# Kernel tuning notes

Hardware: AMD Instinct MI355X
Metric: run time of the kernel (lower is better)

## Reference

```python
import jax, jax.numpy as jnp
import numpy as np

N = 35709   # vertices
F = 70789   # triangles
B = 64
CAMERA_DISTANCE = 10.0
FOCAL = 1015.0
IMAGE_SIZE = 224

SH_A = (np.pi, 2 * np.pi / np.sqrt(3.0), 2 * np.pi / np.sqrt(8.0))
SH_C = (1 / np.sqrt(4 * np.pi), np.sqrt(3.0) / np.sqrt(4 * np.pi), 3 * np.sqrt(5.0) / np.sqrt(12 * np.pi))


def _persc_proj():
    center = IMAGE_SIZE / 2
    m = np.array([FOCAL, 0, center, 0, FOCAL, center, 0, 0, 1], dtype=np.float32).reshape(3, 3).T
    return jnp.asarray(m)


def setup_inputs() -> dict:
    key = jax.random.key(0)
    ks = jax.random.split(key, 9)
    return {
        "coeffs": jax.random.normal(ks[0], (B, 257), jnp.float32),
        "meanshape": jax.random.normal(ks[1], (3 * N,), jnp.float32),
        "idBase": jax.random.normal(ks[2], (3 * N, 80), jnp.float32),
        "exBase": jax.random.normal(ks[3], (3 * N, 64), jnp.float32),
        "meantex": jax.random.uniform(ks[4], (3 * N,), jnp.float32) * 255.0,
        "texBase": jax.random.normal(ks[5], (3 * N, 80), jnp.float32),
        "persc_proj": _persc_proj(),
        "init_lit": jnp.array([0.8, 0, 0, 0, 0, 0, 0, 0, 0], jnp.float32).reshape(1, 1, 9),
        "point_buf": jax.random.randint(ks[6], (N, 8), 0, F + 1),   # index F = zero-pad row
        "face_buf": jax.random.randint(ks[7], (F, 3), 0, N),
        "keypoints": jax.random.randint(ks[8], (68,), 0, N),
    }


def _l2norm(x):
    # matches torch F.normalize(p=2, eps=1e-12)
    return x / jnp.maximum(jnp.linalg.norm(x, axis=-1, keepdims=True), 1e-12)


def _rotation(angles):
    x, y, z = angles[:, 0], angles[:, 1], angles[:, 2]
    o, zr = jnp.ones_like(x), jnp.zeros_like(x)
    cx, sx = jnp.cos(x), jnp.sin(x)
    cy, sy = jnp.cos(y), jnp.sin(y)
    cz, sz = jnp.cos(z), jnp.sin(z)
    rx = jnp.stack([o, zr, zr, zr, cx, -sx, zr, sx, cx], -1).reshape(-1, 3, 3)
    ry = jnp.stack([cy, zr, sy, zr, o, zr, -sy, zr, cy], -1).reshape(-1, 3, 3)
    rz = jnp.stack([cz, -sz, zr, sz, cz, zr, zr, zr, o], -1).reshape(-1, 3, 3)
    return jnp.transpose(rz @ ry @ rx, (0, 2, 1))


def _compute_norm(face_shape, face_buf, point_buf):
    tri = face_shape[:, face_buf]                 # (B, F, 3verts, 3xyz) gather
    e1 = tri[:, :, 0] - tri[:, :, 1]
    e2 = tri[:, :, 1] - tri[:, :, 2]
    fn = _l2norm(jnp.cross(e1, e2))               # (B, F, 3)
    fn = jnp.concatenate([fn, jnp.zeros((fn.shape[0], 1, 3), fn.dtype)], axis=1)
    vn = jnp.sum(fn[:, point_buf], axis=2)        # (B, N, 3) gather-sum over 8 faces
    return _l2norm(vn)


def _compute_color(face_texture, face_norm, gamma, init_lit):
    a, c = SH_A, SH_C
    g = gamma.reshape(gamma.shape[0], 3, 9) + init_lit   # (B, 3, 9)
    g = jnp.transpose(g, (0, 2, 1))                      # (B, 9, 3)
    nx, ny, nz = face_norm[..., 0:1], face_norm[..., 1:2], face_norm[..., 2:3]
    Y = jnp.concatenate([
        a[0] * c[0] * jnp.ones_like(nx),
        -a[1] * c[1] * ny,
        a[1] * c[1] * nz,
        -a[1] * c[1] * nx,
        a[2] * c[2] * nx * ny,
        -a[2] * c[2] * ny * nz,
        0.5 * a[2] * c[2] / np.sqrt(3.0) * (3 * nz ** 2 - 1),
        -a[2] * c[2] * nx * nz,
        0.5 * a[2] * c[2] * (nx ** 2 - ny ** 2)], axis=-1)   # (B, N, 9)
    rgb = jnp.einsum('bnk,bkc->bnc', Y, g)
    return rgb * face_texture


def reference(coeffs, meanshape, idBase, exBase, meantex, texBase, persc_proj, init_lit, point_buf, face_buf, keypoints):
    id_c, ex_c, tex_c = coeffs[:, 0:80], coeffs[:, 80:144], coeffs[:, 144:224]
    angles, gamma, trans = coeffs[:, 224:227], coeffs[:, 227:254], coeffs[:, 254:257]
    Bsz = coeffs.shape[0]
    # shape blending (dense GEMMs)
    shape_flat = (jnp.einsum('ij,aj->ai', idBase, id_c)
                  + jnp.einsum('ij,aj->ai', exBase, ex_c)
                  + meanshape[None])
    face_shape = shape_flat.reshape(Bsz, -1, 3)
    rot = _rotation(angles)
    face_shape_t = face_shape @ rot + trans[:, None, :]
    # to camera: z -> camera_distance - z
    face_vertex = jnp.concatenate([face_shape_t[..., :2], CAMERA_DISTANCE - face_shape_t[..., 2:]], axis=-1)
    # perspective projection
    proj = face_vertex @ persc_proj
    face_proj = proj[..., :2] / proj[..., 2:]
    landmark = face_proj[:, keypoints, :]
    # texture blending
    face_texture = ((jnp.einsum('ij,aj->ai', texBase, tex_c) + meantex[None]) / 255.0).reshape(Bsz, -1, 3)
    # mesh normals on untransformed shape, rotated into camera frame
    face_norm = _compute_norm(face_shape, face_buf, point_buf)
    face_norm_r = face_norm @ rot
    face_color = _compute_color(face_texture, face_norm_r, gamma, init_lit)
    return face_vertex, face_color, landmark
```

## Files before the change

kernel.cpp:

```cpp
#include <hip/hip_runtime.h>

#define N_V 35709
#define N_F 70789
#define NR  (3*N_V)
#define NB  64

#define WS_ROT    0
#define WS_GM     576
#define WS_CTRS   2304
#define WS_CTRT   11520
#define WS_SHAPET 16640

__global__ __launch_bounds__(64) void k_setup_rot(
    const float* __restrict__ coeffs, const float* __restrict__ init_lit,
    float* __restrict__ rotM, float* __restrict__ gm)
{
    int b = threadIdx.x;
    const float* cb = coeffs + b * 257;

    float ax = cb[224], ay = cb[225], az = cb[226];
    float cx = cosf(ax), sx = sinf(ax);
    float cy = cosf(ay), sy = sinf(ay);
    float cz = cosf(az), sz = sinf(az);
    float m[9];
    m[0] = cz * cy;
    m[1] = cz * sy * sx - sz * cx;
    m[2] = sz * sx + cz * sy * cx;
    m[3] = sz * cy;
    m[4] = cz * cx + sz * sy * sx;
    m[5] = sz * sy * cx - cz * sx;
    m[6] = -sy;
    m[7] = cy * sx;
    m[8] = cy * cx;
#pragma unroll
    for (int k = 0; k < 9; k++) rotM[b * 9 + k] = m[k];

#pragma unroll
    for (int k = 0; k < 9; k++) {
        float il = init_lit[k];
#pragma unroll
        for (int c = 0; c < 3; c++)
            gm[b * 27 + k * 3 + c] = cb[227 + c * 9 + k] + il;
    }
}

__global__ __launch_bounds__(64) void k_transpose(
    const float* __restrict__ coeffs,
    float* __restrict__ ctrS, float* __restrict__ ctrT)
{
    int j = blockIdx.x;
    int b = threadIdx.x;
    float v = coeffs[b * 257 + j];
    if (j < 144) ctrS[j * 64 + b] = v;
    else         ctrT[(j - 144) * 64 + b] = v;
}

__global__ __launch_bounds__(256) void k_gemm(
    const float* __restrict__ idBase, const float* __restrict__ exBase,
    const float* __restrict__ texBase, const float* __restrict__ meanshape,
    const float* __restrict__ meantex,
    const float* __restrict__ ctrS, const float* __restrict__ ctrT,
    float* __restrict__ shapeT,
    float* __restrict__ texT,
    int tex_transposed)
{
    __shared__ float tsh[4][64 * 33];
    int w    = threadIdx.x >> 6;
    int lane = threadIdx.x & 63;
    int h    = blockIdx.y;
    int i0w  = blockIdx.x * 256 + w * 64;
    int i    = i0w + lane;
    int iv   = (i < NR) ? i : (NR - 1);
    float* sh = tsh[w];

    float acc[32];

#pragma unroll
    for (int c = 0; c < 32; c++) acc[c] = 0.f;
    {
        const float4* r4 = (const float4*)(idBase + (size_t)iv * 80);
#pragma unroll 2
        for (int jq = 0; jq < 20; jq++) {
            float4 a4 = r4[jq];
            float as[4] = {a4.x, a4.y, a4.z, a4.w};
#pragma unroll
            for (int s = 0; s < 4; s++) {
                float a = as[s];
                const float4* cp = (const float4*)(ctrS + (jq * 4 + s) * 64 + h * 32);
#pragma unroll
                for (int q = 0; q < 8; q++) {
                    float4 c = cp[q];
                    acc[4 * q + 0] += a * c.x;
                    acc[4 * q + 1] += a * c.y;
                    acc[4 * q + 2] += a * c.z;
                    acc[4 * q + 3] += a * c.w;
                }
            }
        }
        const float4* e4 = (const float4*)(exBase + (size_t)iv * 64);
#pragma unroll 2
        for (int jq = 0; jq < 16; jq++) {
            float4 a4 = e4[jq];
            float as[4] = {a4.x, a4.y, a4.z, a4.w};
#pragma unroll
            for (int s = 0; s < 4; s++) {
                float a = as[s];
                const float4* cp = (const float4*)(ctrS + (80 + jq * 4 + s) * 64 + h * 32);
#pragma unroll
                for (int q = 0; q < 8; q++) {
                    float4 c = cp[q];
                    acc[4 * q + 0] += a * c.x;
                    acc[4 * q + 1] += a * c.y;
                    acc[4 * q + 2] += a * c.z;
                    acc[4 * q + 3] += a * c.w;
                }
            }
        }
        float ms = meanshape[iv];
#pragma unroll
        for (int c = 0; c < 32; c++) sh[lane * 33 + c] = acc[c] + ms;
#pragma unroll 4
        for (int it = 0; it < 32; it++) {
            int r  = it * 2 + (lane >> 5);
            int cb = lane & 31;
            int rg = i0w + r;
            float v = sh[r * 33 + cb];
            if (rg < NR) shapeT[(size_t)rg * 64 + h * 32 + cb] = v;
        }
    }

#pragma unroll
    for (int c = 0; c < 32; c++) acc[c] = 0.f;
    {
        const float4* t4 = (const float4*)(texBase + (size_t)iv * 80);
#pragma unroll 2
        for (int jq = 0; jq < 20; jq++) {
            float4 a4 = t4[jq];
            float as[4] = {a4.x, a4.y, a4.z, a4.w};
#pragma unroll
            for (int s = 0; s < 4; s++) {
                float a = as[s];
                const float4* cp = (const float4*)(ctrT + (jq * 4 + s) * 64 + h * 32);
#pragma unroll
                for (int q = 0; q < 8; q++) {
                    float4 c = cp[q];
                    acc[4 * q + 0] += a * c.x;
                    acc[4 * q + 1] += a * c.y;
                    acc[4 * q + 2] += a * c.z;
                    acc[4 * q + 3] += a * c.w;
                }
            }
        }
        float mt = meantex[iv];
        const float inv255 = 1.0f / 255.0f;
        if (tex_transposed) {
#pragma unroll
            for (int c = 0; c < 32; c++) sh[lane * 33 + c] = (acc[c] + mt) * inv255;
#pragma unroll 4
            for (int it = 0; it < 32; it++) {
                int r  = it * 2 + (lane >> 5);
                int cb = lane & 31;
                int rg = i0w + r;
                float v = sh[r * 33 + cb];
                if (rg < NR) texT[(size_t)rg * 64 + h * 32 + cb] = v;
            }
        } else {
            if (i < NR) {
#pragma unroll
                for (int c = 0; c < 32; c++)
                    texT[(size_t)(h * 32 + c) * NR + i] = (acc[c] + mt) * inv255;
            }
        }
    }
}

__global__ __launch_bounds__(256) void k_repack3(
    const float* __restrict__ shapeT, float* __restrict__ shape3)
{
    int wave = threadIdx.x >> 6;
    int b    = threadIdx.x & 63;
    int v0   = blockIdx.x * 32 + wave * 8;
#pragma unroll
    for (int r = 0; r < 8; r++) {
        int v = v0 + r;
        if (v < N_V) {
            float x = shapeT[(size_t)(3 * v)     * 64 + b];
            float y = shapeT[(size_t)(3 * v + 1) * 64 + b];
            float z = shapeT[(size_t)(3 * v + 2) * 64 + b];
            float* o = shape3 + ((size_t)v * 64 + b) * 3;
            o[0] = x; o[1] = y; o[2] = z;
        }
    }
}

__global__ __launch_bounds__(256) void k_facenorm3(
    const float* __restrict__ shape3,
    const int* __restrict__ face_buf,
    float* __restrict__ fnT3)
{
    int wave = threadIdx.x >> 6;
    int b    = threadIdx.x & 63;
    int f0   = blockIdx.x * 32 + wave * 8;
#pragma unroll
    for (int fr = 0; fr < 8; fr++) {
        int f = f0 + fr;
        if (f < N_F) {
            int i0 = face_buf[f * 3 + 0];
            int i1 = face_buf[f * 3 + 1];
            int i2 = face_buf[f * 3 + 2];
            const float* p0 = shape3 + ((size_t)i0 * 64 + b) * 3;
            const float* p1 = shape3 + ((size_t)i1 * 64 + b) * 3;
            const float* p2 = shape3 + ((size_t)i2 * 64 + b) * 3;
            float p0x = p0[0], p0y = p0[1], p0z = p0[2];
            float p1x = p1[0], p1y = p1[1], p1z = p1[2];
            float p2x = p2[0], p2y = p2[1], p2z = p2[2];
            float e1x = p0x - p1x, e1y = p0y - p1y, e1z = p0z - p1z;
            float e2x = p1x - p2x, e2y = p1y - p2y, e2z = p1z - p2z;
            float ccx = e1y * e2z - e1z * e2y;
            float ccy = e1z * e2x - e1x * e2z;
            float ccz = e1x * e2y - e1y * e2x;
            float l = sqrtf(ccx * ccx + ccy * ccy + ccz * ccz);
            float inv = 1.0f / fmaxf(l, 1e-12f);
            float* o = fnT3 + ((size_t)f * 64 + b) * 3;
            o[0] = ccx * inv; o[1] = ccy * inv; o[2] = ccz * inv;
        } else if (f == N_F) {
            float* o = fnT3 + ((size_t)f * 64 + b) * 3;
            o[0] = 0.f; o[1] = 0.f; o[2] = 0.f;
        }
    }
}

__global__ __launch_bounds__(256) void k_facenorm(
    const float* __restrict__ shapeT,
    const int* __restrict__ face_buf,
    float* __restrict__ fnT3)
{
    int wave = threadIdx.x >> 6;
    int b    = threadIdx.x & 63;
    int f0   = blockIdx.x * 32 + wave * 8;
#pragma unroll
    for (int fr = 0; fr < 8; fr++) {
        int f = f0 + fr;
        if (f < N_F) {
            int i0 = face_buf[f * 3 + 0];
            int i1 = face_buf[f * 3 + 1];
            int i2 = face_buf[f * 3 + 2];
            float p0x = shapeT[(size_t)(3 * i0)     * 64 + b];
            float p0y = shapeT[(size_t)(3 * i0 + 1) * 64 + b];
            float p0z = shapeT[(size_t)(3 * i0 + 2) * 64 + b];
            float p1x = shapeT[(size_t)(3 * i1)     * 64 + b];
            float p1y = shapeT[(size_t)(3 * i1 + 1) * 64 + b];
            float p1z = shapeT[(size_t)(3 * i1 + 2) * 64 + b];
            float p2x = shapeT[(size_t)(3 * i2)     * 64 + b];
            float p2y = shapeT[(size_t)(3 * i2 + 1) * 64 + b];
            float p2z = shapeT[(size_t)(3 * i2 + 2) * 64 + b];
            float e1x = p0x - p1x, e1y = p0y - p1y, e1z = p0z - p1z;
            float e2x = p1x - p2x, e2y = p1y - p2y, e2z = p1z - p2z;
            float ccx = e1y * e2z - e1z * e2y;
            float ccy = e1z * e2x - e1x * e2z;
            float ccz = e1x * e2y - e1y * e2x;
            float l = sqrtf(ccx * ccx + ccy * ccy + ccz * ccz);
            float inv = 1.0f / fmaxf(l, 1e-12f);
            float* o = fnT3 + ((size_t)f * 64 + b) * 3;
            o[0] = ccx * inv; o[1] = ccy * inv; o[2] = ccz * inv;
        } else if (f == N_F) {
            float* o = fnT3 + ((size_t)f * 64 + b) * 3;
            o[0] = 0.f; o[1] = 0.f; o[2] = 0.f;
        }
    }
}

__global__ __launch_bounds__(256) void k_vertex_fn(
    const float* __restrict__ shapeT,
    const float* __restrict__ texT,
    const float* __restrict__ fnT3,
    const float* __restrict__ rotM, const float* __restrict__ gm,
    const float* __restrict__ coeffs,
    const int* __restrict__ point_buf,
    float* __restrict__ out_vertex, float* __restrict__ out_color)
{
    __shared__ float sh[64 * 49];
    int wave = threadIdx.x >> 6;
    int b    = threadIdx.x & 63;
    int v0   = blockIdx.x * 16;
    int nvalid = N_V - v0; if (nvalid > 16) nvalid = 16;
    int kmax = 3 * nvalid;

    float m0 = rotM[b * 9 + 0], m1 = rotM[b * 9 + 1], m2 = rotM[b * 9 + 2];
    float m3 = rotM[b * 9 + 3], m4 = rotM[b * 9 + 4], m5 = rotM[b * 9 + 5];
    float m6 = rotM[b * 9 + 6], m7 = rotM[b * 9 + 7], m8 = rotM[b * 9 + 8];
    float tx = coeffs[b * 257 + 254], ty = coeffs[b * 257 + 255], tz = coeffs[b * 257 + 256];
    float g[27];
#pragma unroll
    for (int k = 0; k < 27; k++) g[k] = gm[b * 27 + k];

    const float A0C0 = 0.8862269254527580f;
    const float A1C1 = 1.7724538509055159f;
    const float A2C2 = 2.4270323912f;
    const float C6   = 0.7006239022f;
    const float C8   = 1.2135161956f;

    int pf[4][8];
    float sxv[4], syv[4], szv[4];
    float t0v[4], t1v[4], t2v[4];
#pragma unroll
    for (int vr = 0; vr < 4; vr++) {
        int v = v0 + wave * 4 + vr;
        int vc = (v < N_V) ? v : (N_V - 1);
#pragma unroll
        for (int k = 0; k < 8; k++) pf[vr][k] = point_buf[vc * 8 + k];
        sxv[vr] = shapeT[(size_t)(3 * vc)     * 64 + b];
        syv[vr] = shapeT[(size_t)(3 * vc + 1) * 64 + b];
        szv[vr] = shapeT[(size_t)(3 * vc + 2) * 64 + b];
        t0v[vr] = texT[(size_t)(3 * vc)     * 64 + b];
        t1v[vr] = texT[(size_t)(3 * vc + 1) * 64 + b];
        t2v[vr] = texT[(size_t)(3 * vc + 2) * 64 + b];
    }

    float vert[4][3];
    float col[4][3];

#pragma unroll
    for (int vr = 0; vr < 4; vr++) {
        float fx[8], fy[8], fz[8];
#pragma unroll
        for (int k = 0; k < 8; k++) {
            const float* fp = fnT3 + ((size_t)pf[vr][k] * 64 + b) * 3;
            fx[k] = fp[0]; fy[k] = fp[1]; fz[k] = fp[2];
        }

        float vx = m0 * sxv[vr] + m1 * syv[vr] + m2 * szv[vr] + tx;
        float vy = m3 * sxv[vr] + m4 * syv[vr] + m5 * szv[vr] + ty;
        float vz = m6 * sxv[vr] + m7 * syv[vr] + m8 * szv[vr] + tz;
        vert[vr][0] = vx; vert[vr][1] = vy; vert[vr][2] = 10.0f - vz;

        float nx = 0.f, ny = 0.f, nz = 0.f;
#pragma unroll
        for (int k = 0; k < 8; k++) { nx += fx[k]; ny += fy[k]; nz += fz[k]; }
        float l = sqrtf(nx * nx + ny * ny + nz * nz);
        float inv = 1.0f / fmaxf(l, 1e-12f);
        nx *= inv; ny *= inv; nz *= inv;

        float rx = m0 * nx + m1 * ny + m2 * nz;
        float ry = m3 * nx + m4 * ny + m5 * nz;
        float rz = m6 * nx + m7 * ny + m8 * nz;

        float Y0 = A0C0;
        float Y1 = -A1C1 * ry;
        float Y2 =  A1C1 * rz;
        float Y3 = -A1C1 * rx;
        float Y4 =  A2C2 * rx * ry;
        float Y5 = -A2C2 * ry * rz;
        float Y6 =  C6 * (3.f * rz * rz - 1.f);
        float Y7 = -A2C2 * rx * rz;
        float Y8 =  C8 * (rx * rx - ry * ry);

        float tex3[3] = {t0v[vr], t1v[vr], t2v[vr]};
#pragma unroll
        for (int c = 0; c < 3; c++) {
            float rgb = Y0 * g[0 + c] + Y1 * g[3 + c] + Y2 * g[6 + c] + Y3 * g[9 + c] +
                        Y4 * g[12 + c] + Y5 * g[15 + c] + Y6 * g[18 + c] + Y7 * g[21 + c] +
                        Y8 * g[24 + c];
            col[vr][c] = rgb * tex3[c];
        }
    }

#pragma unroll
    for (int vr = 0; vr < 4; vr++)
#pragma unroll
        for (int c = 0; c < 3; c++)
            sh[b * 49 + (wave * 4 + vr) * 3 + c] = vert[vr][c];
    __syncthreads();
#pragma unroll 4
    for (int it = 0; it < 12; it++) {
        int f = it * 256 + threadIdx.x;
        int bb = f / 48, k = f - bb * 48;
        if (k < kmax)
            __builtin_nontemporal_store(sh[bb * 49 + k],
                                        out_vertex + (size_t)bb * NR + 3 * (size_t)v0 + k);
    }
    __syncthreads();

#pragma unroll
    for (int vr = 0; vr < 4; vr++)
#pragma unroll
        for (int c = 0; c < 3; c++)
            sh[b * 49 + (wave * 4 + vr) * 3 + c] = col[vr][c];
    __syncthreads();
#pragma unroll 4
    for (int it = 0; it < 12; it++) {
        int f = it * 256 + threadIdx.x;
        int bb = f / 48, k = f - bb * 48;
        if (k < kmax)
            __builtin_nontemporal_store(sh[bb * 49 + k],
                                        out_color + (size_t)bb * NR + 3 * (size_t)v0 + k);
    }
}

__global__ __launch_bounds__(256) void k_vertex(
    const float* __restrict__ shapeT,
    const float* __restrict__ texT,
    const float* __restrict__ rotM, const float* __restrict__ gm,
    const float* __restrict__ coeffs,
    const int* __restrict__ point_buf, const int* __restrict__ face_buf,
    float* __restrict__ out_vertex, float* __restrict__ out_color,
    int tex_in_out)
{
    __shared__ float sh[64 * 97];
    int wave = threadIdx.x >> 6;
    int b    = threadIdx.x & 63;
    int v0   = blockIdx.x * 32;
    int nvalid = N_V - v0; if (nvalid > 32) nvalid = 32;
    int kmax = 3 * nvalid;

    float m0 = rotM[b * 9 + 0], m1 = rotM[b * 9 + 1], m2 = rotM[b * 9 + 2];
    float m3 = rotM[b * 9 + 3], m4 = rotM[b * 9 + 4], m5 = rotM[b * 9 + 5];
    float m6 = rotM[b * 9 + 6], m7 = rotM[b * 9 + 7], m8 = rotM[b * 9 + 8];
    float tx = coeffs[b * 257 + 254], ty = coeffs[b * 257 + 255], tz = coeffs[b * 257 + 256];
    float g[27];
#pragma unroll
    for (int k = 0; k < 27; k++) g[k] = gm[b * 27 + k];

    const float A0C0 = 0.8862269254527580f;
    const float A1C1 = 1.7724538509055159f;
    const float A2C2 = 2.4270323912f;
    const float C6   = 0.7006239022f;
    const float C8   = 1.2135161956f;

    float vert[8][3];
    float col[8][3];

#pragma unroll
    for (int vr = 0; vr < 8; vr++) {
        int v = v0 + wave * 8 + vr;
        bool valid = (v < N_V);
        int vc = valid ? v : (N_V - 1);

        float sx0 = shapeT[(size_t)(3 * vc)     * 64 + b];
        float sy0 = shapeT[(size_t)(3 * vc + 1) * 64 + b];
        float sz0 = shapeT[(size_t)(3 * vc + 2) * 64 + b];

        float vx = m0 * sx0 + m1 * sy0 + m2 * sz0 + tx;
        float vy = m3 * sx0 + m4 * sy0 + m5 * sz0 + ty;
        float vz = m6 * sx0 + m7 * sy0 + m8 * sz0 + tz;
        vert[vr][0] = vx; vert[vr][1] = vy; vert[vr][2] = 10.0f - vz;

        float nx = 0.f, ny = 0.f, nz = 0.f;
#pragma unroll
        for (int k = 0; k < 8; k++) {
            int f = point_buf[vc * 8 + k];
            if (f < N_F) {
                int i0 = face_buf[f * 3], i1 = face_buf[f * 3 + 1], i2 = face_buf[f * 3 + 2];
                float p0x = shapeT[(size_t)(3 * i0)     * 64 + b];
                float p0y = shapeT[(size_t)(3 * i0 + 1) * 64 + b];
                float p0z = shapeT[(size_t)(3 * i0 + 2) * 64 + b];
                float p1x = shapeT[(size_t)(3 * i1)     * 64 + b];
                float p1y = shapeT[(size_t)(3 * i1 + 1) * 64 + b];
                float p1z = shapeT[(size_t)(3 * i1 + 2) * 64 + b];
                float p2x = shapeT[(size_t)(3 * i2)     * 64 + b];
                float p2y = shapeT[(size_t)(3 * i2 + 1) * 64 + b];
                float p2z = shapeT[(size_t)(3 * i2 + 2) * 64 + b];
                float e1x = p0x - p1x, e1y = p0y - p1y, e1z = p0z - p1z;
                float e2x = p1x - p2x, e2y = p1y - p2y, e2z = p1z - p2z;
                float ccx = e1y * e2z - e1z * e2y;
                float ccy = e1z * e2x - e1x * e2z;
                float ccz = e1x * e2y - e1y * e2x;
                float l = sqrtf(ccx * ccx + ccy * ccy + ccz * ccz);
                float inv = 1.0f / fmaxf(l, 1e-12f);
                nx += ccx * inv; ny += ccy * inv; nz += ccz * inv;
            }
        }
        float l = sqrtf(nx * nx + ny * ny + nz * nz);
        float inv = 1.0f / fmaxf(l, 1e-12f);
        nx *= inv; ny *= inv; nz *= inv;

        float rx = m0 * nx + m1 * ny + m2 * nz;
        float ry = m3 * nx + m4 * ny + m5 * nz;
        float rz = m6 * nx + m7 * ny + m8 * nz;

        float Y0 = A0C0;
        float Y1 = -A1C1 * ry;
        float Y2 =  A1C1 * rz;
        float Y3 = -A1C1 * rx;
        float Y4 =  A2C2 * rx * ry;
        float Y5 = -A2C2 * ry * rz;
        float Y6 =  C6 * (3.f * rz * rz - 1.f);
        float Y7 = -A2C2 * rx * rz;
        float Y8 =  C8 * (rx * rx - ry * ry);

        float t0, t1, t2;
        if (tex_in_out) {
            size_t ob = (size_t)b * NR + 3 * (size_t)vc;
            t0 = out_color[ob]; t1 = out_color[ob + 1]; t2 = out_color[ob + 2];
        } else {
            t0 = texT[(size_t)(3 * vc)     * 64 + b];
            t1 = texT[(size_t)(3 * vc + 1) * 64 + b];
            t2 = texT[(size_t)(3 * vc + 2) * 64 + b];
        }
        float tex3[3] = {t0, t1, t2};
#pragma unroll
        for (int c = 0; c < 3; c++) {
            float rgb = Y0 * g[0 + c] + Y1 * g[3 + c] + Y2 * g[6 + c] + Y3 * g[9 + c] +
                        Y4 * g[12 + c] + Y5 * g[15 + c] + Y6 * g[18 + c] + Y7 * g[21 + c] +
                        Y8 * g[24 + c];
            col[vr][c] = rgb * tex3[c];
        }
    }

#pragma unroll
    for (int vr = 0; vr < 8; vr++)
#pragma unroll
        for (int c = 0; c < 3; c++)
            sh[b * 97 + (wave * 8 + vr) * 3 + c] = vert[vr][c];
    __syncthreads();
#pragma unroll 4
    for (int it = 0; it < 24; it++) {
        int f = it * 256 + threadIdx.x;
        int bb = f / 96, k = f - bb * 96;
        if (k < kmax)
            __builtin_nontemporal_store(sh[bb * 97 + k],
                                        out_vertex + (size_t)bb * NR + 3 * (size_t)v0 + k);
    }
    __syncthreads();

#pragma unroll
    for (int vr = 0; vr < 8; vr++)
#pragma unroll
        for (int c = 0; c < 3; c++)
            sh[b * 97 + (wave * 8 + vr) * 3 + c] = col[vr][c];
    __syncthreads();
#pragma unroll 4
    for (int it = 0; it < 24; it++) {
        int f = it * 256 + threadIdx.x;
        int bb = f / 96, k = f - bb * 96;
        if (k < kmax)
            __builtin_nontemporal_store(sh[bb * 97 + k],
                                        out_color + (size_t)bb * NR + 3 * (size_t)v0 + k);
    }
}

__global__ __launch_bounds__(64) void k_landmark(
    const float* __restrict__ shapeT, const int* __restrict__ keypoints,
    const float* __restrict__ rotM, const float* __restrict__ coeffs,
    const float* __restrict__ P,
    float* __restrict__ out_lm)
{
    int l = blockIdx.x;
    int b = threadIdx.x;
    int kp = keypoints[l];

    float m0 = rotM[b * 9 + 0], m1 = rotM[b * 9 + 1], m2 = rotM[b * 9 + 2];
    float m3 = rotM[b * 9 + 3], m4 = rotM[b * 9 + 4], m5 = rotM[b * 9 + 5];
    float m6 = rotM[b * 9 + 6], m7 = rotM[b * 9 + 7], m8 = rotM[b * 9 + 8];
    float tx = coeffs[b * 257 + 254], ty = coeffs[b * 257 + 255], tz = coeffs[b * 257 + 256];

    float sx0 = shapeT[(size_t)(3 * kp)     * 64 + b];
    float sy0 = shapeT[(size_t)(3 * kp + 1) * 64 + b];
    float sz0 = shapeT[(size_t)(3 * kp + 2) * 64 + b];

    float x = m0 * sx0 + m1 * sy0 + m2 * sz0 + tx;
    float y = m3 * sx0 + m4 * sy0 + m5 * sz0 + ty;
    float z = 10.0f - (m6 * sx0 + m7 * sy0 + m8 * sz0 + tz);

    float p0 = x * P[0] + y * P[3] + z * P[6];
    float p1 = x * P[1] + y * P[4] + z * P[7];
    float p2 = x * P[2] + y * P[5] + z * P[8];

    size_t o = ((size_t)b * 68 + l) * 2;
    out_lm[o]     = p0 / p2;
    out_lm[o + 1] = p1 / p2;
}

extern "C" void kernel_launch(void* const* d_in, const int* in_sizes, int n_in,
                              void* d_out, int out_size, void* d_ws, size_t ws_size,
                              hipStream_t stream) {
    const float* coeffs    = (const float*)d_in[0];
    const float* meanshape = (const float*)d_in[1];
    const float* idBase    = (const float*)d_in[2];
    const float* exBase    = (const float*)d_in[3];
    const float* meantex   = (const float*)d_in[4];
    const float* texBase   = (const float*)d_in[5];
    const float* persc     = (const float*)d_in[6];
    const float* init_lit  = (const float*)d_in[7];
    const int*   point_buf = (const int*)d_in[8];
    const int*   face_buf  = (const int*)d_in[9];
    const int*   keypoints = (const int*)d_in[10];

    float* ws = (float*)d_ws;
    float* rotM   = ws + WS_ROT;
    float* gm     = ws + WS_GM;
    float* ctrS   = ws + WS_CTRS;
    float* ctrT   = ws + WS_CTRT;
    float* shapeT = ws + WS_SHAPET;

    float* out_vertex = (float*)d_out;
    float* out_color  = out_vertex + (size_t)NB * NR;
    float* out_lm     = out_color  + (size_t)NB * NR;

    size_t NRx64   = (size_t)NR * 64;
    size_t fn3_len = (size_t)(N_F + 1) * 64 * 3;
    size_t sh3_len = (size_t)N_V * 64 * 3;

    size_t need_tex = ((size_t)WS_SHAPET + 2 * NRx64) * sizeof(float);
    size_t need_fn  = need_tex + fn3_len * sizeof(float);
    size_t need_s3  = need_fn + sh3_len * sizeof(float);

    int tex_transposed = (ws_size >= need_tex) ? 1 : 0;
    int use_fn         = (ws_size >= need_fn) ? 1 : 0;
    int use_s3         = (ws_size >= need_s3) ? 1 : 0;

    float* texT   = tex_transposed ? (shapeT + NRx64) : out_color;
    float* fnT3   = shapeT + 2 * NRx64;
    float* shape3 = fnT3 + fn3_len;

    k_setup_rot<<<1, 64, 0, stream>>>(coeffs, init_lit, rotM, gm);
    k_transpose<<<224, 64, 0, stream>>>(coeffs, ctrS, ctrT);

    dim3 gg((NR + 255) / 256, 2);
    k_gemm<<<gg, 256, 0, stream>>>(idBase, exBase, texBase, meanshape,
                                   meantex, ctrS, ctrT, shapeT, texT,
                                   tex_transposed);

    if (use_fn) {
        int fb = (N_F + 1 + 31) / 32;
        if (use_s3) {
            int rb = (N_V + 31) / 32;
            k_repack3<<<rb, 256, 0, stream>>>(shapeT, shape3);
            k_facenorm3<<<fb, 256, 0, stream>>>(shape3, face_buf, fnT3);
        } else {
            k_facenorm<<<fb, 256, 0, stream>>>(shapeT, face_buf, fnT3);
        }
        int vb = (N_V + 15) / 16;
        k_vertex_fn<<<vb, 256, 0, stream>>>(shapeT, texT, fnT3, rotM, gm, coeffs,
                                            point_buf, out_vertex, out_color);
    } else {
        int vb = (N_V + 31) / 32;
        k_vertex<<<vb, 256, 0, stream>>>(shapeT, tex_transposed ? texT : nullptr,
                                         rotM, gm, coeffs, point_buf, face_buf,
                                         out_vertex, out_color,
                                         tex_transposed ? 0 : 1);
    }

    k_landmark<<<68, 64, 0, stream>>>(shapeT, keypoints, rotM, coeffs, persc, out_lm);
}
```

Before: 296.3 us.

## Restructure blending GEMM: lane per batch, LDS-staged coefficients, 16 rows per wave

The blending GEMM now maps each lane to one batch element and each wave to 16 consecutive basis rows, instead of one lane per row with 32 batch accumulators split over two grid halves. Coefficients are staged once per block in LDS, and basis rows are loaded as wave-uniform float4 broadcasts. Outputs are written directly in row-major 64-wide form, which removes the LDS transpose and the duplicated basis reads across the two grid halves. The trade-off is more block barriers and uniform scalar-like loads of basis rows, which may make the loads latency-bound.

Result: slower. 411.5 us (+38.9%).

```diff
diff --git a/kernel.cpp b/kernel.cpp
--- a/kernel.cpp
+++ b/kernel.cpp
@@ -64,111 +64,118 @@
     float* __restrict__ texT,
     int tex_transposed)
 {
-    __shared__ float tsh[4][64 * 33];
-    int w    = threadIdx.x >> 6;
-    int lane = threadIdx.x & 63;
-    int h    = blockIdx.y;
-    int i0w  = blockIdx.x * 256 + w * 64;
-    int i    = i0w + lane;
-    int iv   = (i < NR) ? i : (NR - 1);
-    float* sh = tsh[w];
-
-    float acc[32];
-
-#pragma unroll
-    for (int c = 0; c < 32; c++) acc[c] = 0.f;
+    __shared__ float lds[80 * 64];
+    const int t    = threadIdx.x;
+    const int lane = t & 63;
+    const int wu   = __builtin_amdgcn_readfirstlane((int)(threadIdx.x >> 6));
+    const int r0   = blockIdx.x * 64 + wu * 16;
+
+    float acc[16];
+#pragma unroll
+    for (int k = 0; k < 16; k++) acc[k] = 0.f;
+
     {
-        const float4* r4 = (const float4*)(idBase + (size_t)iv * 80);
+        const float4* s4 = (const float4*)ctrS;
+        float4* d4 = (float4*)lds;
+#pragma unroll
+        for (int k = 0; k < 5; k++) d4[t + k * 256] = s4[t + k * 256];
+    }
+    __syncthreads();
 #pragma unroll 2
-        for (int jq = 0; jq < 20; jq++) {
-            float4 a4 = r4[jq];
-            float as[4] = {a4.x, a4.y, a4.z, a4.w};
-#pragma unroll
-            for (int s = 0; s < 4; s++) {
-                float a = as[s];
-                const float4* cp = (const float4*)(ctrS + (jq * 4 + s) * 64 + h * 32);
-#pragma unroll
-                for (int q = 0; q < 8; q++) {
-                    float4 c = cp[q];
-                    acc[4 * q + 0] += a * c.x;
-                    acc[4 * q + 1] += a * c.y;
-                    acc[4 * q + 2] += a * c.z;
-                    acc[4 * q + 3] += a * c.w;
-                }
+    for (int jc = 0; jc < 80; jc += 4) {
+        float4 a[16];
+#pragma unroll
+        for (int k = 0; k < 16; k++) {
+            int r = r0 + k; if (r > NR - 1) r = NR - 1;
+            a[k] = *(const float4*)(idBase + (size_t)r * 80 + jc);
+        }
+#pragma unroll
+        for (int jj = 0; jj < 4; jj++) {
+            float c = lds[(jc + jj) * 64 + lane];
+#pragma unroll
+            for (int k = 0; k < 16; k++)
+                acc[k] += ((const float*)&a[k])[jj] * c;
+        }
+    }
+    __syncthreads();
+
+    {
+        const float4* s4 = (const float4*)(ctrS + 80 * 64);
+        float4* d4 = (float4*)lds;
+#pragma unroll
+        for (int k = 0; k < 4; k++) d4[t + k * 256] = s4[t + k * 256];
+    }
+    __syncthreads();
+#pragma unroll 2
+    for (int jc = 0; jc < 64; jc += 4) {
+        float4 a[16];
+#pragma unroll
+        for (int k = 0; k < 16; k++) {
+            int r = r0 + k; if (r > NR - 1) r = NR - 1;
+            a[k] = *(const float4*)(exBase + (size_t)r * 64 + jc);
+        }
+#pragma unroll
+        for (int jj = 0; jj < 4; jj++) {
+            float c = lds[(jc + jj) * 64 + lane];
+#pragma unroll
+            for (int k = 0; k < 16; k++)
+                acc[k] += ((const float*)&a[k])[jj] * c;
+        }
+    }
+
+#pragma unroll
+    for (int k = 0; k < 16; k++) {
+        int r = r0 + k;
+        if (r < NR) {
+            float ms = meanshape[r];
+            shapeT[(size_t)r * 64 + lane] = acc[k] + ms;
+        }
+    }
+    __syncthreads();
+
+    {
+        const float4* s4 = (const float4*)ctrT;
+        float4* d4 = (float4*)lds;
+#pragma unroll
+        for (int k = 0; k < 5; k++) d4[t + k * 256] = s4[t + k * 256];
+    }
+    __syncthreads();
+#pragma unroll
+    for (int k = 0; k < 16; k++) acc[k] = 0.f;
+#pragma unroll 2
+    for (int jc = 0; jc < 80; jc += 4) {
+        float4 a[16];
+#pragma unroll
+        for (int k = 0; k < 16; k++) {
+            int r = r0 + k; if (r > NR - 1) r = NR - 1;
+            a[k] = *(const float4*)(texBase + (size_t)r * 80 + jc);
+        }
+#pragma unroll
+        for (int jj = 0; jj < 4; jj++) {
+            float c = lds[(jc + jj) * 64 + lane];
+#pragma unroll
+            for (int k = 0; k < 16; k++)
+                acc[k] += ((const float*)&a[k])[jj] * c;
+        }
+    }
+
+    const float inv255 = 1.0f / 255.0f;
+    if (tex_transposed) {
+#pragma unroll
+        for (int k = 0; k < 16; k++) {
+            int r = r0 + k;
+            if (r < NR) {
+                float mt = meantex[r];
+                texT[(size_t)r * 64 + lane] = (acc[k] + mt) * inv255;
             }
         }
-        const float4* e4 = (const float4*)(exBase + (size_t)iv * 64);
-#pragma unroll 2
-        for (int jq = 0; jq < 16; jq++) {
-            float4 a4 = e4[jq];
-            float as[4] = {a4.x, a4.y, a4.z, a4.w};
-#pragma unroll
-            for (int s = 0; s < 4; s++) {
-                float a = as[s];
-                const float4* cp = (const float4*)(ctrS + (80 + jq * 4 + s) * 64 + h * 32);
-#pragma unroll
-                for (int q = 0; q < 8; q++) {
-                    float4 c = cp[q];
-                    acc[4 * q + 0] += a * c.x;
-                    acc[4 * q + 1] += a * c.y;
-                    acc[4 * q + 2] += a * c.z;
-                    acc[4 * q + 3] += a * c.w;
-                }
-            }
-        }
-        float ms = meanshape[iv];
-#pragma unroll
-        for (int c = 0; c < 32; c++) sh[lane * 33 + c] = acc[c] + ms;
-#pragma unroll 4
-        for (int it = 0; it < 32; it++) {
-            int r  = it * 2 + (lane >> 5);
-            int cb = lane & 31;
-            int rg = i0w + r;
-            float v = sh[r * 33 + cb];
-            if (rg < NR) shapeT[(size_t)rg * 64 + h * 32 + cb] = v;
-        }
-    }
-
-#pragma unroll
-    for (int c = 0; c < 32; c++) acc[c] = 0.f;
-    {
-        const float4* t4 = (const float4*)(texBase + (size_t)iv * 80);
-#pragma unroll 2
-        for (int jq = 0; jq < 20; jq++) {
-            float4 a4 = t4[jq];
-            float as[4] = {a4.x, a4.y, a4.z, a4.w};
-#pragma unroll
-            for (int s = 0; s < 4; s++) {
-                float a = as[s];
-                const float4* cp = (const float4*)(ctrT + (jq * 4 + s) * 64 + h * 32);
-#pragma unroll
-                for (int q = 0; q < 8; q++) {
-                    float4 c = cp[q];
-                    acc[4 * q + 0] += a * c.x;
-                    acc[4 * q + 1] += a * c.y;
-                    acc[4 * q + 2] += a * c.z;
-                    acc[4 * q + 3] += a * c.w;
-                }
-            }
-        }
-        float mt = meantex[iv];
-        const float inv255 = 1.0f / 255.0f;
-        if (tex_transposed) {
-#pragma unroll
-            for (int c = 0; c < 32; c++) sh[lane * 33 + c] = (acc[c] + mt) * inv255;
-#pragma unroll 4
-            for (int it = 0; it < 32; it++) {
-                int r  = it * 2 + (lane >> 5);
-                int cb = lane & 31;
-                int rg = i0w + r;
-                float v = sh[r * 33 + cb];
-                if (rg < NR) texT[(size_t)rg * 64 + h * 32 + cb] = v;
-            }
-        } else {
-            if (i < NR) {
-#pragma unroll
-                for (int c = 0; c < 32; c++)
-                    texT[(size_t)(h * 32 + c) * NR + i] = (acc[c] + mt) * inv255;
+    } else {
+#pragma unroll
+        for (int k = 0; k < 16; k++) {
+            int r = r0 + k;
+            if (r < NR) {
+                float mt = meantex[r];
+                texT[(size_t)lane * NR + r] = (acc[k] + mt) * inv255;
             }
         }
     }
@@ -616,8 +623,8 @@
     k_setup_rot<<<1, 64, 0, stream>>>(coeffs, init_lit, rotM, gm);
     k_transpose<<<224, 64, 0, stream>>>(coeffs, ctrS, ctrT);
 
-    dim3 gg((NR + 255) / 256, 2);
-    k_gemm<<<gg, 256, 0, stream>>>(idBase, exBase, texBase, meanshape,
+    int gb = (NR + 63) / 64;
+    k_gemm<<<gb, 256, 0, stream>>>(idBase, exBase, texBase, meanshape,
                                    meantex, ctrS, ctrT, shapeT, texT,
                                    tex_transposed);
 
```
